# Performance work log

Measured on AMD Instinct MI355X. Metric: run time of the kernel, lower is better.

Reference implementation:

```python
import jax, jax.numpy as jnp
import numpy as np

N, D = 8192, 256

def setup_inputs() -> dict:
    key = jax.random.key(0)
    k1, k2 = jax.random.split(key)
    data = jnp.zeros((1,), dtype=jnp.float32)  # unused by the module
    Z = jax.random.normal(k1, (N, D), dtype=jnp.float32)
    A_hat = jax.random.uniform(k2, (N, N), dtype=jnp.float32)
    return {"data": data, "Z": Z, "A_hat": A_hat}

def reference(data, Z, A_hat):
    A = A_hat.astype(jnp.float32)
    # D^{-1/2} A D^{-1/2}: diagonal matmuls are mathematically row/col scaling
    d_inv_sqrt = 1.0 / jnp.sqrt(A.sum(axis=1) + 1e-10)  # [N]
    A_norm = A * d_inv_sqrt[:, None] * d_inv_sqrt[None, :]  # [N, N]
    # cosine similarity (F.normalize uses eps=1e-12 clamp on the norm)
    z_norm = jnp.linalg.norm(Z, axis=1, keepdims=True)
    Z_n = Z / jnp.maximum(z_norm, 1e-12)
    similarity = Z_n @ Z_n.T  # [N, N]
    homo_loss = -jnp.sum(A_norm * similarity)
    hetero_loss = jnp.sum((1.0 - A_norm) * similarity)
    return (homo_loss, hetero_loss)
```

## Files before the change

kernel.cpp:

```cpp
#include <hip/hip_runtime.h>
#include <hip/hip_fp16.h>

typedef _Float16 f16x8 __attribute__((ext_vector_type(8)));
typedef _Float16 f16x4 __attribute__((ext_vector_type(4)));
typedef float    f32x4 __attribute__((ext_vector_type(4)));

constexpr int Nn = 8192;
constexpr int Dd = 256;

constexpr int BM = 64;
constexpr int KC = 1024;
constexpr int SK = 64;
constexpr int NSC = KC / SK;

__global__ __launch_bounds__(256) void k_rowsum(const float* __restrict__ A,
                                                float* __restrict__ dis,
                                                float* __restrict__ rd,
                                                float* __restrict__ T) {
    if (blockIdx.x == 0 && threadIdx.x == 0) *T = 0.f;
    const int row  = blockIdx.x * 4 + (threadIdx.x >> 6);
    const int lane = threadIdx.x & 63;
    const float4* rp = reinterpret_cast<const float4*>(A + (size_t)row * Nn);
    float s = 0.f;
    #pragma unroll
    for (int i = 0; i < Nn / 256; ++i) {
        float4 v = rp[i * 64 + lane];
        s += (v.x + v.y) + (v.z + v.w);
    }
    #pragma unroll
    for (int off = 32; off > 0; off >>= 1) s += __shfl_down(s, off, 64);
    if (lane == 0) {
        float rs = s + 1e-10f;
        dis[row] = rsqrtf(rs);
        rd[row]  = sqrtf(rs);
    }
}

__global__ __launch_bounds__(256) void k_makeYt(const float* __restrict__ Z,
                                               const float* __restrict__ dis,
                                               _Float16* __restrict__ Yt,
                                               _Float16* __restrict__ Yr) {
    __shared__ float nrm[64][4];
    __shared__ _Float16 tile[Dd][72];
    const int t = threadIdx.x;
    const int r = t >> 2, q = t & 3;
    const int row = blockIdx.x * 64 + r;
    const float4* zp = reinterpret_cast<const float4*>(Z + (size_t)row * Dd + q * 64);
    float4 v[16];
    float ss = 0.f;
    #pragma unroll
    for (int i = 0; i < 16; ++i) {
        v[i] = zp[i];
        ss += v[i].x*v[i].x + v[i].y*v[i].y + v[i].z*v[i].z + v[i].w*v[i].w;
    }
    nrm[r][q] = ss;
    __syncthreads();
    const float tot   = nrm[r][0] + nrm[r][1] + nrm[r][2] + nrm[r][3];
    const float scale = dis[row] / fmaxf(sqrtf(tot), 1e-12f);
    #pragma unroll
    for (int i = 0; i < 16; ++i) {
        const int c0 = q * 64 + i * 4;
        f16x4 y = { (_Float16)(v[i].x * scale), (_Float16)(v[i].y * scale),
                    (_Float16)(v[i].z * scale), (_Float16)(v[i].w * scale) };
        tile[c0+0][r] = y[0];
        tile[c0+1][r] = y[1];
        tile[c0+2][r] = y[2];
        tile[c0+3][r] = y[3];
        *reinterpret_cast<f16x4*>(Yr + (size_t)row * Dd + c0) = y;
    }
    __syncthreads();
    int4*       dst = reinterpret_cast<int4*>(Yt + (size_t)t * Nn + blockIdx.x * 64);
    const int4* src = reinterpret_cast<const int4*>(&tile[t][0]);
    #pragma unroll
    for (int i = 0; i < 8; ++i) dst[i] = src[i];
}

__global__ __launch_bounds__(256) void k_colsum(const _Float16* __restrict__ Yt,
                                                const float* __restrict__ rd,
                                                float* __restrict__ s) {
    const int k = blockIdx.x;
    const int t = threadIdx.x;
    const _Float16* yp = Yt + (size_t)k * Nn + t * 32;
    const float*    rp = rd + t * 32;
    float acc = 0.f;
    #pragma unroll
    for (int i = 0; i < 32; ++i) acc += (float)yp[i] * rp[i];
    #pragma unroll
    for (int off = 32; off > 0; off >>= 1) acc += __shfl_down(acc, off, 64);
    __shared__ float red[4];
    if ((t & 63) == 0) red[t >> 6] = acc;
    __syncthreads();
    if (t == 0) s[k] = red[0] + red[1] + red[2] + red[3];
}

__global__ __launch_bounds__(512, 4) void k_main(const float* __restrict__ A,
                                                 const _Float16* __restrict__ Yt,
                                                 const _Float16* __restrict__ Yr,
                                                 float* __restrict__ T) {
    __shared__ _Float16 Ys[2 * Dd * SK];

    const int ib = blockIdx.x & (Nn / BM - 1);
    const int jb = blockIdx.x >> 7;
    const int I0 = ib * BM;
    const int K0 = jb * KC;
    const int w  = threadIdx.x >> 6;
    const int wr = w >> 1;
    const int wn = w & 1;
    const int l  = threadIdx.x & 63;
    const int lr = l & 15;
    const int lk = l >> 4;

    const size_t arow = (size_t)(I0 + wr * 16 + lr) * Nn;

    f32x4 acc[8];
    #pragma unroll
    for (int t = 0; t < 8; ++t) acc[t] = f32x4{0.f, 0.f, 0.f, 0.f};

    #define STAGE(SC, BUF)                                                     \
    {   const int kc = K0 + (SC) * SK;                                         \
        _Pragma("unroll")                                                      \
        for (int q = 0; q < 4; ++q) {                                          \
            const int nrow = w * 32 + q * 8 + (l >> 3);                        \
            const int s8   = (l & 7) ^ (l >> 3);                               \
            __builtin_amdgcn_global_load_lds(                                  \
                (const __attribute__((address_space(1))) unsigned int*)        \
                    (Yt + (size_t)nrow * Nn + kc + s8 * 8),                    \
                (__attribute__((address_space(3))) unsigned int*)              \
                    (Ys + (BUF) * (Dd * SK) + (w * 32 + q * 8) * SK),          \
                16, 0, 0);                                                     \
        }                                                                      \
    }

    float4 av[4];
    #define LOADA(SC)                                                          \
    {   const float* ab = A + arow + K0 + (SC) * SK + lk * 8;                  \
        av[0] = *reinterpret_cast<const float4*>(ab);                          \
        av[1] = *reinterpret_cast<const float4*>(ab + 4);                      \
        av[2] = *reinterpret_cast<const float4*>(ab + 32);                     \
        av[3] = *reinterpret_cast<const float4*>(ab + 36);                     \
    }

    STAGE(0, 0);
    LOADA(0);
    asm volatile("s_waitcnt vmcnt(0)" ::: "memory");
    __builtin_amdgcn_s_barrier();

    for (int sc = 0; sc < NSC; ++sc) {
        const int cur = sc & 1;
        f16x8 af[2];
        #pragma unroll
        for (int ks = 0; ks < 2; ++ks) {
            const float4 a0 = av[ks*2], a1 = av[ks*2+1];
            af[ks] = f16x8{ (_Float16)a0.x, (_Float16)a0.y, (_Float16)a0.z, (_Float16)a0.w,
                            (_Float16)a1.x, (_Float16)a1.y, (_Float16)a1.z, (_Float16)a1.w };
        }
        if (sc + 1 < NSC) {
            STAGE(sc + 1, cur ^ 1);
            LOADA(sc + 1);
        }
        #pragma unroll
        for (int tn = 0; tn < 8; ++tn) {
            const int n = wn * 128 + tn * 16 + lr;
            #pragma unroll
            for (int ks = 0; ks < 2; ++ks) {
                const int sl = (ks * 4 + lk) ^ (lr & 7);
                const f16x8 bf = *reinterpret_cast<const f16x8*>(
                    Ys + cur * (Dd * SK) + n * SK + sl * 8);
                acc[tn] = __builtin_amdgcn_mfma_f32_16x16x32_f16(af[ks], bf, acc[tn], 0, 0, 0);
            }
        }
        if (sc + 1 < NSC) {
            asm volatile("s_waitcnt vmcnt(4)" ::: "memory");
            __builtin_amdgcn_s_barrier();
        }
    }

    float part = 0.f;
    #pragma unroll
    for (int tn = 0; tn < 8; ++tn) {
        const int n = wn * 128 + tn * 16 + lr;
        #pragma unroll
        for (int r = 0; r < 4; ++r) {
            const int i = I0 + wr * 16 + lk * 4 + r;
            part += acc[tn][r] * (float)Yr[(size_t)i * Dd + n];
        }
    }
    #pragma unroll
    for (int off = 32; off > 0; off >>= 1) part += __shfl_down(part, off, 64);
    __shared__ float red[8];
    if (l == 0) red[w] = part;
    __syncthreads();
    if (threadIdx.x == 0) {
        float t = 0.f;
        #pragma unroll
        for (int i = 0; i < 8; ++i) t += red[i];
        atomicAdd(T, t);
    }
}

__global__ __launch_bounds__(256) void k_final(const float* __restrict__ s,
                                               const float* __restrict__ T,
                                               float* __restrict__ out) {
    const int t = threadIdx.x;
    float v = s[t];
    float p = v * v;
    #pragma unroll
    for (int off = 32; off > 0; off >>= 1) p += __shfl_down(p, off, 64);
    __shared__ float red[4];
    if ((t & 63) == 0) red[t >> 6] = p;
    __syncthreads();
    if (t == 0) {
        const float ss = red[0] + red[1] + red[2] + red[3];
        const float Tv = *T;
        out[0] = -Tv;
        out[1] = ss - Tv;
    }
}

extern "C" void kernel_launch(void* const* d_in, const int* in_sizes, int n_in,
                              void* d_out, int out_size, void* d_ws, size_t ws_size,
                              hipStream_t stream) {
    const float* Z = (const float*)d_in[1];
    const float* A = (const float*)d_in[2];
    float* out = (float*)d_out;

    char* ws = (char*)d_ws;
    float*    dis = (float*)(ws);
    float*    rd  = (float*)(ws + 32768);
    float*    s   = (float*)(ws + 65536);
    float*    T   = (float*)(ws + 66560);
    _Float16* Yt  = (_Float16*)(ws + 131072);
    _Float16* Yr  = (_Float16*)(ws + 131072 + (size_t)Nn * Dd * 2);

    k_rowsum<<<Nn / 4, 256, 0, stream>>>(A, dis, rd, T);
    k_makeYt<<<Nn / 64, 256, 0, stream>>>(Z, dis, Yt, Yr);
    k_colsum<<<Dd, 256, 0, stream>>>(Yt, rd, s);
    k_main<<<(Nn / BM) * (Nn / KC), 512, 0, stream>>>(A, Yt, Yr, T);
    k_final<<<1, 256, 0, stream>>>(s, T, out);
}
```

Baseline: 151.1 us.

## Switch main GEMM to 32x32x16 MFMA with split-K warp layout

Replaces the 16x16x32 MFMA tiling with 32x32x16 MFMA instructions. The eight waves are rearranged into 2 (M) x 2 (N) x 2 (K-half) instead of 4 (M) x 2 (N). Each wave now covers half of every 64-wide K chunk, and the partial results are combined in the existing block-level sum. The aim is fewer LDS fragment reads and fewer MFMA issues per FLOP. The epilogue row mapping is updated to the 32x32 accumulator layout, and the A loads are re-offset to match.

Result: no change. 148.2 us (-1.9%).

```diff
diff --git a/kernel.cpp b/kernel.cpp
--- a/kernel.cpp
+++ b/kernel.cpp
@@ -1,9 +1,9 @@
 #include <hip/hip_runtime.h>
 #include <hip/hip_fp16.h>
 
-typedef _Float16 f16x8 __attribute__((ext_vector_type(8)));
-typedef _Float16 f16x4 __attribute__((ext_vector_type(4)));
-typedef float    f32x4 __attribute__((ext_vector_type(4)));
+typedef _Float16 f16x8  __attribute__((ext_vector_type(8)));
+typedef _Float16 f16x4  __attribute__((ext_vector_type(4)));
+typedef float    f32x16 __attribute__((ext_vector_type(16)));
 
 constexpr int Nn = 8192;
 constexpr int Dd = 256;
@@ -103,18 +103,20 @@
     const int jb = blockIdx.x >> 7;
     const int I0 = ib * BM;
     const int K0 = jb * KC;
-    const int w  = threadIdx.x >> 6;
-    const int wr = w >> 1;
-    const int wn = w & 1;
-    const int l  = threadIdx.x & 63;
-    const int lr = l & 15;
-    const int lk = l >> 4;
-
-    const size_t arow = (size_t)(I0 + wr * 16 + lr) * Nn;
-
-    f32x4 acc[8];
-    #pragma unroll
-    for (int t = 0; t < 8; ++t) acc[t] = f32x4{0.f, 0.f, 0.f, 0.f};
+    const int w   = threadIdx.x >> 6;
+    const int wm  = w & 1;
+    const int wn  = (w >> 1) & 1;
+    const int wk  = w >> 2;
+    const int l   = threadIdx.x & 63;
+    const int ln  = l & 31;
+    const int lkh = l >> 5;
+
+    const size_t arow = (size_t)(I0 + wm * 32 + ln) * Nn;
+    const int    koff = wk * 32 + lkh * 8;
+
+    f32x16 acc[4];
+    #pragma unroll
+    for (int t = 0; t < 4; ++t) acc[t] = (f32x16)(0.f);
 
     #define STAGE(SC, BUF)                                                     \
     {   const int kc = K0 + (SC) * SK;                                         \
@@ -133,11 +135,11 @@
 
     float4 av[4];
     #define LOADA(SC)                                                          \
-    {   const float* ab = A + arow + K0 + (SC) * SK + lk * 8;                  \
+    {   const float* ab = A + arow + K0 + (SC) * SK + koff;                    \
         av[0] = *reinterpret_cast<const float4*>(ab);                          \
         av[1] = *reinterpret_cast<const float4*>(ab + 4);                      \
-        av[2] = *reinterpret_cast<const float4*>(ab + 32);                     \
-        av[3] = *reinterpret_cast<const float4*>(ab + 36);                     \
+        av[2] = *reinterpret_cast<const float4*>(ab + 16);                     \
+        av[3] = *reinterpret_cast<const float4*>(ab + 20);                     \
     }
 
     STAGE(0, 0);
@@ -159,14 +161,14 @@
             LOADA(sc + 1);
         }
         #pragma unroll
-        for (int tn = 0; tn < 8; ++tn) {
-            const int n = wn * 128 + tn * 16 + lr;
+        for (int tn = 0; tn < 4; ++tn) {
+            const int n = wn * 128 + tn * 32 + ln;
             #pragma unroll
             for (int ks = 0; ks < 2; ++ks) {
-                const int sl = (ks * 4 + lk) ^ (lr & 7);
+                const int sl = (wk * 4 + ks * 2 + lkh) ^ (n & 7);
                 const f16x8 bf = *reinterpret_cast<const f16x8*>(
                     Ys + cur * (Dd * SK) + n * SK + sl * 8);
-                acc[tn] = __builtin_amdgcn_mfma_f32_16x16x32_f16(af[ks], bf, acc[tn], 0, 0, 0);
+                acc[tn] = __builtin_amdgcn_mfma_f32_32x32x16_f16(af[ks], bf, acc[tn], 0, 0, 0);
             }
         }
         if (sc + 1 < NSC) {
@@ -177,11 +179,11 @@
 
     float part = 0.f;
     #pragma unroll
-    for (int tn = 0; tn < 8; ++tn) {
-        const int n = wn * 128 + tn * 16 + lr;
-        #pragma unroll
-        for (int r = 0; r < 4; ++r) {
-            const int i = I0 + wr * 16 + lk * 4 + r;
+    for (int tn = 0; tn < 4; ++tn) {
+        const int n = wn * 128 + tn * 32 + ln;
+        #pragma unroll
+        for (int r = 0; r < 16; ++r) {
+            const int i = I0 + wm * 32 + (r & 3) + 8 * (r >> 2) + 4 * lkh;
             part += acc[tn][r] * (float)Yr[(size_t)i * Dd + n];
         }
     }
```
